# Kernel optimization log

Hardware: AMD Instinct MI355X
Metric: run time of the kernel (lower is better)

The kernel has to match this reference:

```python
import jax, jax.numpy as jnp
import numpy as np

N_PIX = 4_194_304      # native emulator wavelength grid length
N_BINS = 350_000       # number of data wavelength bins (searchsorted labels)
MEDIAN_WL = 10500.0    # Angstroms, np.median(wl_bin_edges)
C_KMS = 299792.458     # speed of light, km/s
PI_SRC = 3.1415926654  # the (slightly off) pi literal used in the source
KERNEL_TAPS = 901      # torch.arange(-4.5, 4.51, 0.01)


def _conv_same(flux, kernel):
    """conv1d with padding='same'; kernels are symmetric so corr == conv."""
    half = kernel.shape[0] // 2
    out = jax.lax.conv_general_dilated(
        flux[None, None, :], kernel[None, None, :],
        window_strides=(1,), padding=[(half, half)])
    return out[0, 0]


def setup_inputs() -> dict:
    key = jax.random.key(0)
    k1, k2 = jax.random.split(key)
    return {
        "high_res_model": jax.random.uniform(k1, (N_PIX,), dtype=jnp.float32),
        "ln_sigma_angs": jnp.asarray(-2.3, dtype=jnp.float32),
        "ln_vsini": jnp.asarray(2.89, dtype=jnp.float32),
        "segment_ids": jnp.sort(jax.random.randint(k2, (N_PIX,), 0, N_BINS)),
    }


def reference(high_res_model, ln_sigma_angs, ln_vsini, segment_ids):
    dt = high_res_model.dtype
    grid = jnp.linspace(-4.5, 4.5, KERNEL_TAPS).astype(dt)
    sigma_angs = 0.01 + jnp.exp(ln_sigma_angs)
    vsini = 0.9 + jnp.exp(ln_vsini)

    # --- rotational broadening kernel ---
    x = (C_KMS * grid / MEDIAN_WL) / vsini
    x2 = jnp.minimum(x * x, 1.0)                     # torch.clamp(x2, max=1)
    inside = x2 < 0.99999999
    safe_x2 = jnp.where(inside, x2, 0.0)             # avoid sqrt(neg)/nan-grad
    rot_kernel = jnp.where(inside, 2.0 * jnp.sqrt(1.0 - safe_x2), 0.0)
    rot_kernel = rot_kernel / jnp.sum(rot_kernel)
    rot = _conv_same(high_res_model, rot_kernel)

    # --- instrumental (Gaussian) broadening kernel ---
    gauss = (1.0 / (sigma_angs * jnp.sqrt(jnp.asarray(2.0 * PI_SRC, dt)))
             * jnp.exp(-0.5 * grid * grid / (sigma_angs * sigma_angs)) * 0.01)
    conv = _conv_same(rot, gauss)

    # --- resample to data: fused segment mean (replaces split+per-bin mean) ---
    sums = jax.ops.segment_sum(conv, segment_ids, num_segments=N_BINS)
    counts = jax.ops.segment_sum(jnp.ones_like(conv), segment_ids,
                                 num_segments=N_BINS)
    means = sums / jnp.maximum(counts, 1.0)
    return jnp.clip(means, 0.0, 1.0)[1:-1]
```

## Files before the change

### kernel.cpp

```cpp
#include <hip/hip_runtime.h>
#include <hip/hip_bf16.h>

#define TAPS 901
#define CB 256
#define R 15
#define NGRP 16
#define NK (R * NGRP)
#define OPB (CB * R)
#define TILE 4112

__device__ __forceinline__ float4 ld4(const float* p) {
  return *reinterpret_cast<const float4*>(p);
}

__global__ __launch_bounds__(1024) void prep(
    const float* __restrict__ lns, const float* __restrict__ lnv,
    const float* __restrict__ flux, const int* __restrict__ ids,
    float* __restrict__ comb_w, int* __restrict__ bounds,
    float* __restrict__ sums, int n) {
  __shared__ float rk[1024], gk[1024], red[1024];
  __shared__ float ck[2048];
  __shared__ int sb[8];
  const int t = threadIdx.x;
  if (t < 8) sb[t] = (t & 1) ? -1 : 4096;
  __syncthreads();

  const float sigma = 0.01f + expf(lns[0]);
  const float vsini = 0.9f + expf(lnv[0]);

  float rv = 0.f, gv = 0.f;
  if (t < TAPS) {
    float g = -4.5f + 0.01f * (float)t;
    float x = (299792.458f * g / 10500.0f) / vsini;
    float x2 = fminf(x * x, 1.0f);
    if (x2 < 1.0f) rv = 2.0f * sqrtf(1.0f - x2);
    gv = (1.0f / (sigma * sqrtf(2.0f * 3.1415926654f))) *
         expf(-0.5f * g * g / (sigma * sigma)) * 0.01f;
  }
  red[t] = rv;
  __syncthreads();
  for (int s = 512; s > 0; s >>= 1) {
    if (t < s) red[t] += red[t + s];
    __syncthreads();
  }
  const float rsum = red[0];

  const float rw = (t < TAPS) ? rv / rsum : 0.f;
  rk[t] = rw;
  gk[t] = gv;
  if (t < TAPS) {
    if (rw != 0.f)          { atomicMin(&sb[0], t); atomicMax(&sb[1], t); }
    if (fabsf(gv) > 1e-10f) { atomicMin(&sb[2], t); atomicMax(&sb[3], t); }
  }
  __syncthreads();
  const int rlo = sb[0], rhi = sb[1], glo = sb[2], ghi = sb[3];
  int flo = 450 - glo; if (flo < 0) flo = 0;
  int fhi = ghi - 450; if (fhi < 0) fhi = 0;

  if (blockIdx.x == 0) {
    for (int t2 = t; t2 < 2048; t2 += 1024) {
      float c = 0.f;
      if (t2 <= 1800) {
        int jmin = rlo > t2 - ghi ? rlo : t2 - ghi;
        int jmax = rhi < t2 - glo ? rhi : t2 - glo;
        for (int j = jmin; j <= jmax; ++j) c += rk[j] * gk[t2 - j];
      }
      ck[t2] = c;
      comb_w[t2] = c;
      if (t2 <= 1800 && fabsf(c) > 1e-12f) { atomicMin(&sb[4], t2); atomicMax(&sb[5], t2); }
    }
    __syncthreads();
    if (t == 0) {
      int clo = sb[4], chi = sb[5];
      if (chi < clo) { clo = 900; chi = 900; }
      while (chi - (clo & ~3) + 1 > NK) {
        if (fabsf(ck[clo]) <= fabsf(ck[chi])) ++clo; else --chi;
      }
      bounds[0] = clo & ~3; bounds[1] = flo; bounds[2] = fhi;
    }
  } else if (blockIdx.x == 1) {
    const int m = flo + fhi;
    float* rbuf = ck;
    for (int j = t; j < m; j += 1024) {
      float s = 0.f;
      int j0 = 450 - j > rlo ? 450 - j : rlo;
      for (int j2 = j0; j2 <= rhi; ++j2) s += rk[j2] * flux[j + j2 - 450];
      rbuf[j] = s;
    }
    __syncthreads();
    for (int i = t; i < flo; i += 1024) {
      float c = 0.f;
      int k0 = 450 - i > glo ? 450 - i : glo;
      for (int k = k0; k <= ghi; ++k) c += gk[k] * rbuf[i + k - 450];
      atomicAdd(&sums[ids[i]], c);
    }
  } else {
    const int m = flo + fhi;
    float* rbuf = ck;
    const int jbase = n - m;
    for (int jj = t; jj < m; jj += 1024) {
      int j = jbase + jj;
      float s = 0.f;
      int j2hi = n - 1 + 450 - j < rhi ? n - 1 + 450 - j : rhi;
      for (int j2 = rlo; j2 <= j2hi; ++j2) s += rk[j2] * flux[j + j2 - 450];
      rbuf[jj] = s;
    }
    __syncthreads();
    for (int ii = t; ii < fhi; ii += 1024) {
      int i = n - fhi + ii;
      float c = 0.f;
      int khi = n - 1 + 450 - i < ghi ? n - 1 + 450 - i : ghi;
      for (int k = glo; k <= khi; ++k) c += gk[k] * rbuf[i + k - 450 - jbase];
      atomicAdd(&sums[ids[i]], c);
    }
  }
}

__global__ __launch_bounds__(CB) void conv_scatter(
    const float* __restrict__ flux, const float* __restrict__ comb_w,
    const int* __restrict__ bounds, const int* __restrict__ ids,
    float* __restrict__ sums, int* __restrict__ bstart, int n, int nbins) {
  __shared__ __align__(16) float lds[TILE];
  __shared__ __align__(16) float wl[NGRP * 16];
  const int tid = threadIdx.x;
  const int clo4 = __builtin_amdgcn_readfirstlane(bounds[0]);
  const int flo  = __builtin_amdgcn_readfirstlane(bounds[1]);
  const int fhi  = __builtin_amdgcn_readfirstlane(bounds[2]);
  const int blockBase = blockIdx.x * OPB;
  const int start = blockBase - 900 + clo4;

  for (int j = tid * 4; j < OPB + NK; j += CB * 4) {
    int g = start + j;
    float4 v;
    if (g >= 0 && g + 3 < n) {
      v = ld4(flux + g);
    } else {
      v.x = (unsigned)g       < (unsigned)n ? flux[g]     : 0.f;
      v.y = (unsigned)(g + 1) < (unsigned)n ? flux[g + 1] : 0.f;
      v.z = (unsigned)(g + 2) < (unsigned)n ? flux[g + 2] : 0.f;
      v.w = (unsigned)(g + 3) < (unsigned)n ? flux[g + 3] : 0.f;
    }
    *reinterpret_cast<float4*>(&lds[j]) = v;
  }
  {
    const int g = tid >> 4, u = tid & 15;
    wl[tid] = (u < 15) ? comb_w[clo4 + g * 15 + u] : 0.f;
  }
  __syncthreads();

  const int idx0 = tid * R;
  float win[R];
#pragma unroll
  for (int r = 0; r < R; ++r) win[r] = lds[idx0 + r];
  float acc[R];
#pragma unroll
  for (int r = 0; r < R; ++r) acc[r] = 0.f;

  const float4* wl4 = reinterpret_cast<const float4*>(wl);
#define TAP(u, wv)                                                     \
  {                                                                    \
    _Pragma("unroll") for (int r = 0; r < R; ++r)                      \
        acc[r] = fmaf(wv, win[((u) + r) % R], acc[r]);                 \
    win[u] = lds[idx0 + kk + (u) + R];                                 \
  }
#pragma unroll 2
  for (int g = 0; g < NGRP; ++g) {
    const int kk = g * R;
    const float4 q0 = wl4[g * 4 + 0];
    const float4 q1 = wl4[g * 4 + 1];
    const float4 q2 = wl4[g * 4 + 2];
    const float4 q3 = wl4[g * 4 + 3];
    TAP(0, q0.x)  TAP(1, q0.y)  TAP(2, q0.z)  TAP(3, q0.w)
    TAP(4, q1.x)  TAP(5, q1.y)  TAP(6, q1.z)  TAP(7, q1.w)
    TAP(8, q2.x)  TAP(9, q2.y)  TAP(10, q2.z) TAP(11, q2.w)
    TAP(12, q3.x) TAP(13, q3.y) TAP(14, q3.z)
  }
#undef TAP

  const int base = blockBase + idx0;
  const int loskip = flo - base;
  const int hicap = (n - fhi) - base;
  int prev = (base > 0) ? ((base < n) ? ids[base - 1] : 0) : -1;
  int cur = -1; float run = 0.f;
#pragma unroll
  for (int r = 0; r < R; ++r) {
    const int p = base + r;
    if (p < n) {
      const int id = ids[p];
      if (id != prev) {
        for (int b = prev + 1; b <= id; ++b) bstart[b] = p;
        prev = id;
      }
      if (r >= loskip && r < hicap) {
        if (id == cur) {
          run += acc[r];
        } else {
          if (cur >= 0) atomicAdd(&sums[cur], run);
          cur = id; run = acc[r];
        }
      }
    }
  }
  if (cur >= 0) atomicAdd(&sums[cur], run);
  if (base < n && base + R > n - 1) {
    for (int b = prev + 1; b < nbins; ++b) bstart[b] = n;
  }
}

__global__ __launch_bounds__(256) void seg_mean(
    const float* __restrict__ sums, const int* __restrict__ bstart,
    float* __restrict__ out, int out_n) {
  const int gid = blockIdx.x * blockDim.x + threadIdx.x;
  if (gid >= out_n) return;
  const int b = gid + 1;
  const int c = bstart[b + 1] - bstart[b];
  const float mean = sums[b] / (float)(c > 1 ? c : 1);
  out[gid] = fminf(fmaxf(mean, 0.f), 1.f);
}

extern "C" void kernel_launch(void* const* d_in, const int* in_sizes, int n_in,
                              void* d_out, int out_size, void* d_ws,
                              size_t ws_size, hipStream_t stream) {
  const float* flux = (const float*)d_in[0];
  const float* lns  = (const float*)d_in[1];
  const float* lnv  = (const float*)d_in[2];
  const int*   ids  = (const int*)d_in[3];
  float* out = (float*)d_out;
  const int n = in_sizes[0];
  const int nbins = out_size + 2;

  float* ws      = (float*)d_ws;
  float* comb_w  = ws;
  int*   bounds  = (int*)(ws + 2048);
  float* sums    = ws + 2112;
  int*   bstart  = (int*)(sums + nbins);

  hipMemsetAsync(sums, 0, (size_t)nbins * sizeof(float), stream);
  prep<<<3, 1024, 0, stream>>>(lns, lnv, flux, ids, comb_w, bounds, sums, n);
  const int nblk = (n + OPB - 1) / OPB;
  conv_scatter<<<nblk, CB, 0, stream>>>(flux, comb_w, bounds, ids, sums,
                                        bstart, n, nbins);
  seg_mean<<<(out_size + 255) / 256, 256, 0, stream>>>(sums, bstart, out,
                                                       out_size);
}
```

Before: 141.2 us.

## Replace per-pixel convolution with prefix-sum bin dot products per segment

Rather than convolving every pixel and scatter-adding into bins, each block builds a prefix sum of its flux window in shared memory. Each bin's sum of convolved values is then computed directly as a weighted dot product of prefix differences with the combined kernel. This removes the global atomics and the separate mean kernel. Edge corrections are precomputed into a per-bin buffer and bin starts come from a separate kernel. The changes add more kernel launches and a serial chunked scan, and float prefix sums over thousands of elements can lose precision. The cost now scales with bins per block times taps instead of pixels times taps.

```diff
diff --git a/kernel.cpp b/kernel.cpp
--- a/kernel.cpp
+++ b/kernel.cpp
@@ -4,20 +4,14 @@
 #define TAPS 901
 #define CB 256
 #define R 15
-#define NGRP 16
-#define NK (R * NGRP)
+#define NK 240
 #define OPB (CB * R)
-#define TILE 4112
-
-__device__ __forceinline__ float4 ld4(const float* p) {
-  return *reinterpret_cast<const float4*>(p);
-}
-
-__global__ __launch_bounds__(1024) void prep(
+#define WL 4864
+#define CHUNK 19
+
+__global__ __launch_bounds__(1024) void prep0(
     const float* __restrict__ lns, const float* __restrict__ lnv,
-    const float* __restrict__ flux, const int* __restrict__ ids,
-    float* __restrict__ comb_w, int* __restrict__ bounds,
-    float* __restrict__ sums, int n) {
+    float* __restrict__ comb_w, int* __restrict__ bounds) {
   __shared__ float rk[1024], gk[1024], red[1024];
   __shared__ float ck[2048];
   __shared__ int sb[8];
@@ -54,33 +48,74 @@
   }
   __syncthreads();
   const int rlo = sb[0], rhi = sb[1], glo = sb[2], ghi = sb[3];
+
+  for (int t2 = t; t2 < 2048; t2 += 1024) {
+    float c = 0.f;
+    if (t2 <= 1800) {
+      int jmin = rlo > t2 - ghi ? rlo : t2 - ghi;
+      int jmax = rhi < t2 - glo ? rhi : t2 - glo;
+      for (int j = jmin; j <= jmax; ++j) c += rk[j] * gk[t2 - j];
+    }
+    ck[t2] = c;
+    comb_w[t2] = c;
+    if (t2 <= 1800 && fabsf(c) > 1e-12f) { atomicMin(&sb[4], t2); atomicMax(&sb[5], t2); }
+  }
+  __syncthreads();
+  if (t == 0) {
+    int clo = sb[4], chi = sb[5];
+    if (chi < clo) { clo = 900; chi = 900; }
+    while (chi - (clo & ~3) + 1 > NK) {
+      if (fabsf(ck[clo]) <= fabsf(ck[chi])) ++clo; else --chi;
+    }
+    int flo = 450 - glo; if (flo < 0) flo = 0;
+    int fhi = ghi - 450; if (fhi < 0) fhi = 0;
+    bounds[0] = clo & ~3; bounds[1] = flo; bounds[2] = fhi;
+  }
+}
+
+__global__ __launch_bounds__(1024) void prep1(
+    const float* __restrict__ lns, const float* __restrict__ lnv,
+    const float* __restrict__ flux, const int* __restrict__ ids,
+    const float* __restrict__ comb_w, const int* __restrict__ bounds,
+    float* __restrict__ edgeCorr, int n) {
+  __shared__ float rk[1024], gk[1024], red[1024], rbuf[928];
+  __shared__ int sb[4];
+  const int t = threadIdx.x;
+  if (t < 4) sb[t] = (t & 1) ? -1 : 4096;
+  __syncthreads();
+
+  const float sigma = 0.01f + expf(lns[0]);
+  const float vsini = 0.9f + expf(lnv[0]);
+  float rv = 0.f, gv = 0.f;
+  if (t < TAPS) {
+    float g = -4.5f + 0.01f * (float)t;
+    float x = (299792.458f * g / 10500.0f) / vsini;
+    float x2 = fminf(x * x, 1.0f);
+    if (x2 < 1.0f) rv = 2.0f * sqrtf(1.0f - x2);
+    gv = (1.0f / (sigma * sqrtf(2.0f * 3.1415926654f))) *
+         expf(-0.5f * g * g / (sigma * sigma)) * 0.01f;
+  }
+  red[t] = rv;
+  __syncthreads();
+  for (int s = 512; s > 0; s >>= 1) {
+    if (t < s) red[t] += red[t + s];
+    __syncthreads();
+  }
+  const float rsum = red[0];
+  rk[t] = (t < TAPS) ? rv / rsum : 0.f;
+  gk[t] = gv;
+  if (t < TAPS) {
+    if (rk[t] != 0.f)       { atomicMin(&sb[0], t); atomicMax(&sb[1], t); }
+    if (fabsf(gv) > 1e-10f) { atomicMin(&sb[2], t); atomicMax(&sb[3], t); }
+  }
+  __syncthreads();
+  const int rlo = sb[0], rhi = sb[1], glo = sb[2], ghi = sb[3];
   int flo = 450 - glo; if (flo < 0) flo = 0;
   int fhi = ghi - 450; if (fhi < 0) fhi = 0;
+  const int m = flo + fhi;
+  const int clo4 = bounds[0];
 
   if (blockIdx.x == 0) {
-    for (int t2 = t; t2 < 2048; t2 += 1024) {
-      float c = 0.f;
-      if (t2 <= 1800) {
-        int jmin = rlo > t2 - ghi ? rlo : t2 - ghi;
-        int jmax = rhi < t2 - glo ? rhi : t2 - glo;
-        for (int j = jmin; j <= jmax; ++j) c += rk[j] * gk[t2 - j];
-      }
-      ck[t2] = c;
-      comb_w[t2] = c;
-      if (t2 <= 1800 && fabsf(c) > 1e-12f) { atomicMin(&sb[4], t2); atomicMax(&sb[5], t2); }
-    }
-    __syncthreads();
-    if (t == 0) {
-      int clo = sb[4], chi = sb[5];
-      if (chi < clo) { clo = 900; chi = 900; }
-      while (chi - (clo & ~3) + 1 > NK) {
-        if (fabsf(ck[clo]) <= fabsf(ck[chi])) ++clo; else --chi;
-      }
-      bounds[0] = clo & ~3; bounds[1] = flo; bounds[2] = fhi;
-    }
-  } else if (blockIdx.x == 1) {
-    const int m = flo + fhi;
-    float* rbuf = ck;
     for (int j = t; j < m; j += 1024) {
       float s = 0.f;
       int j0 = 450 - j > rlo ? 450 - j : rlo;
@@ -89,14 +124,17 @@
     }
     __syncthreads();
     for (int i = t; i < flo; i += 1024) {
-      float c = 0.f;
+      float ex = 0.f;
       int k0 = 450 - i > glo ? 450 - i : glo;
-      for (int k = k0; k <= ghi; ++k) c += gk[k] * rbuf[i + k - 450];
-      atomicAdd(&sums[ids[i]], c);
+      for (int k = k0; k <= ghi; ++k) ex += gk[k] * rbuf[i + k - 450];
+      float cb = 0.f;
+      for (int t2 = 0; t2 < NK; ++t2) {
+        int q = i + clo4 + t2 - 900;
+        if (q >= 0 && q < n) cb = fmaf(comb_w[clo4 + t2], flux[q], cb);
+      }
+      atomicAdd(&edgeCorr[ids[i]], ex - cb);
     }
   } else {
-    const int m = flo + fhi;
-    float* rbuf = ck;
     const int jbase = n - m;
     for (int jj = t; jj < m; jj += 1024) {
       int j = jbase + jj;
@@ -108,114 +146,113 @@
     __syncthreads();
     for (int ii = t; ii < fhi; ii += 1024) {
       int i = n - fhi + ii;
-      float c = 0.f;
+      float ex = 0.f;
       int khi = n - 1 + 450 - i < ghi ? n - 1 + 450 - i : ghi;
-      for (int k = glo; k <= khi; ++k) c += gk[k] * rbuf[i + k - 450 - jbase];
-      atomicAdd(&sums[ids[i]], c);
-    }
-  }
-}
-
-__global__ __launch_bounds__(CB) void conv_scatter(
+      for (int k = glo; k <= khi; ++k) ex += gk[k] * rbuf[i + k - 450 - jbase];
+      float cb = 0.f;
+      for (int t2 = 0; t2 < NK; ++t2) {
+        int q = i + clo4 + t2 - 900;
+        if (q >= 0 && q < n) cb = fmaf(comb_w[clo4 + t2], flux[q], cb);
+      }
+      atomicAdd(&edgeCorr[ids[i]], ex - cb);
+    }
+  }
+}
+
+__global__ __launch_bounds__(256) void build_bstart(
+    const int* __restrict__ ids, int* __restrict__ bstart, int n, int nbins) {
+  const int gid = blockIdx.x * 256 + threadIdx.x;
+  const int p0 = gid * 8;
+  if (p0 >= n) return;
+  int prev = (p0 == 0) ? -1 : ids[p0 - 1];
+  const int4 a = *reinterpret_cast<const int4*>(ids + p0);
+  const int4 b4 = *reinterpret_cast<const int4*>(ids + p0 + 4);
+  const int v[8] = {a.x, a.y, a.z, a.w, b4.x, b4.y, b4.z, b4.w};
+#pragma unroll
+  for (int r = 0; r < 8; ++r) {
+    const int id = v[r];
+    if (id != prev) {
+      for (int b = prev + 1; b <= id; ++b) bstart[b] = p0 + r;
+      prev = id;
+    }
+  }
+  if (p0 + 8 >= n) {
+    for (int b = prev + 1; b <= nbins; ++b) bstart[b] = n;
+  }
+}
+
+__global__ __launch_bounds__(CB) void bin_dot(
     const float* __restrict__ flux, const float* __restrict__ comb_w,
     const int* __restrict__ bounds, const int* __restrict__ ids,
-    float* __restrict__ sums, int* __restrict__ bstart, int n, int nbins) {
-  __shared__ __align__(16) float lds[TILE];
-  __shared__ __align__(16) float wl[NGRP * 16];
+    const int* __restrict__ bstart, const float* __restrict__ edgeCorr,
+    float* __restrict__ out, int n, int nbins) {
+  __shared__ float W[WL];
+  __shared__ float wl[NK];
+  __shared__ float caux[CB];
   const int tid = threadIdx.x;
   const int clo4 = __builtin_amdgcn_readfirstlane(bounds[0]);
-  const int flo  = __builtin_amdgcn_readfirstlane(bounds[1]);
-  const int fhi  = __builtin_amdgcn_readfirstlane(bounds[2]);
   const int blockBase = blockIdx.x * OPB;
-  const int start = blockBase - 900 + clo4;
-
-  for (int j = tid * 4; j < OPB + NK; j += CB * 4) {
-    int g = start + j;
-    float4 v;
-    if (g >= 0 && g + 3 < n) {
-      v = ld4(flux + g);
+  const int wstart = blockBase - 900 + clo4;
+
+  if (tid == 0) W[0] = 0.f;
+  for (int j = tid; j < WL - 1; j += CB) {
+    const int g = wstart + j;
+    W[1 + j] = ((unsigned)g < (unsigned)n) ? flux[g] : 0.f;
+  }
+  if (tid < NK) wl[tid] = comb_w[clo4 + tid];
+  __syncthreads();
+
+  {
+    const int base = 1 + tid * CHUNK;
+    const int lim = min(base + CHUNK, WL);
+    float s = 0.f;
+    for (int j = base; j < lim; ++j) { s += W[j]; W[j] = s; }
+    caux[tid] = s;
+    __syncthreads();
+    for (int off = 1; off < CB; off <<= 1) {
+      const float v = (tid >= off) ? caux[tid - off] : 0.f;
+      __syncthreads();
+      caux[tid] += v;
+      __syncthreads();
+    }
+    const float offv = (tid == 0) ? 0.f : caux[tid - 1];
+    for (int j = base; j < lim; ++j) W[j] += offv;
+  }
+  __syncthreads();
+
+  const int blo = (blockBase == 0) ? 0 : ids[blockBase - 1] + 1;
+  const int lastpix = min(blockBase + OPB, n) - 1;
+  int bhi = ids[lastpix];
+  if (blockBase + OPB >= n) bhi = nbins - 1;
+  const int oe_last = bstart[bhi + 1] - blockBase;
+  const bool fallback = (oe_last + NK > WL);
+
+  for (int b = blo + tid; b <= bhi; b += CB) {
+    const int s = bstart[b], e = bstart[b + 1];
+    float a0 = 0.f, a1 = 0.f, a2 = 0.f, a3 = 0.f;
+    if (!fallback) {
+      const int os = s - blockBase, oe = e - blockBase;
+#pragma unroll 4
+      for (int t2 = 0; t2 < NK; t2 += 4) {
+        a0 = fmaf(wl[t2 + 0], W[oe + t2 + 0] - W[os + t2 + 0], a0);
+        a1 = fmaf(wl[t2 + 1], W[oe + t2 + 1] - W[os + t2 + 1], a1);
+        a2 = fmaf(wl[t2 + 2], W[oe + t2 + 2] - W[os + t2 + 2], a2);
+        a3 = fmaf(wl[t2 + 3], W[oe + t2 + 3] - W[os + t2 + 3], a3);
+      }
     } else {
-      v.x = (unsigned)g       < (unsigned)n ? flux[g]     : 0.f;
-      v.y = (unsigned)(g + 1) < (unsigned)n ? flux[g + 1] : 0.f;
-      v.z = (unsigned)(g + 2) < (unsigned)n ? flux[g + 2] : 0.f;
-      v.w = (unsigned)(g + 3) < (unsigned)n ? flux[g + 3] : 0.f;
-    }
-    *reinterpret_cast<float4*>(&lds[j]) = v;
-  }
-  {
-    const int g = tid >> 4, u = tid & 15;
-    wl[tid] = (u < 15) ? comb_w[clo4 + g * 15 + u] : 0.f;
-  }
-  __syncthreads();
-
-  const int idx0 = tid * R;
-  float win[R];
-#pragma unroll
-  for (int r = 0; r < R; ++r) win[r] = lds[idx0 + r];
-  float acc[R];
-#pragma unroll
-  for (int r = 0; r < R; ++r) acc[r] = 0.f;
-
-  const float4* wl4 = reinterpret_cast<const float4*>(wl);
-#define TAP(u, wv)                                                     \
-  {                                                                    \
-    _Pragma("unroll") for (int r = 0; r < R; ++r)                      \
-        acc[r] = fmaf(wv, win[((u) + r) % R], acc[r]);                 \
-    win[u] = lds[idx0 + kk + (u) + R];                                 \
-  }
-#pragma unroll 2
-  for (int g = 0; g < NGRP; ++g) {
-    const int kk = g * R;
-    const float4 q0 = wl4[g * 4 + 0];
-    const float4 q1 = wl4[g * 4 + 1];
-    const float4 q2 = wl4[g * 4 + 2];
-    const float4 q3 = wl4[g * 4 + 3];
-    TAP(0, q0.x)  TAP(1, q0.y)  TAP(2, q0.z)  TAP(3, q0.w)
-    TAP(4, q1.x)  TAP(5, q1.y)  TAP(6, q1.z)  TAP(7, q1.w)
-    TAP(8, q2.x)  TAP(9, q2.y)  TAP(10, q2.z) TAP(11, q2.w)
-    TAP(12, q3.x) TAP(13, q3.y) TAP(14, q3.z)
-  }
-#undef TAP
-
-  const int base = blockBase + idx0;
-  const int loskip = flo - base;
-  const int hicap = (n - fhi) - base;
-  int prev = (base > 0) ? ((base < n) ? ids[base - 1] : 0) : -1;
-  int cur = -1; float run = 0.f;
-#pragma unroll
-  for (int r = 0; r < R; ++r) {
-    const int p = base + r;
-    if (p < n) {
-      const int id = ids[p];
-      if (id != prev) {
-        for (int b = prev + 1; b <= id; ++b) bstart[b] = p;
-        prev = id;
-      }
-      if (r >= loskip && r < hicap) {
-        if (id == cur) {
-          run += acc[r];
-        } else {
-          if (cur >= 0) atomicAdd(&sums[cur], run);
-          cur = id; run = acc[r];
+      for (int i = s; i < e; ++i)
+        for (int t2 = 0; t2 < NK; ++t2) {
+          const int q = i + clo4 + t2 - 900;
+          if ((unsigned)q < (unsigned)n) a0 = fmaf(wl[t2], flux[q], a0);
         }
-      }
-    }
-  }
-  if (cur >= 0) atomicAdd(&sums[cur], run);
-  if (base < n && base + R > n - 1) {
-    for (int b = prev + 1; b < nbins; ++b) bstart[b] = n;
-  }
-}
-
-__global__ __launch_bounds__(256) void seg_mean(
-    const float* __restrict__ sums, const int* __restrict__ bstart,
-    float* __restrict__ out, int out_n) {
-  const int gid = blockIdx.x * blockDim.x + threadIdx.x;
-  if (gid >= out_n) return;
-  const int b = gid + 1;
-  const int c = bstart[b + 1] - bstart[b];
-  const float mean = sums[b] / (float)(c > 1 ? c : 1);
-  out[gid] = fminf(fmaxf(mean, 0.f), 1.f);
+    }
+    const float sum = ((a0 + a1) + (a2 + a3)) + edgeCorr[b];
+    if (b >= 1 && b <= nbins - 2) {
+      const int c = e - s;
+      const float mean = sum / (float)(c > 1 ? c : 1);
+      out[b - 1] = fminf(fmaxf(mean, 0.f), 1.f);
+    }
+  }
 }
 
 extern "C" void kernel_launch(void* const* d_in, const int* in_sizes, int n_in,
@@ -229,17 +266,18 @@
   const int n = in_sizes[0];
   const int nbins = out_size + 2;
 
-  float* ws      = (float*)d_ws;
-  float* comb_w  = ws;
-  int*   bounds  = (int*)(ws + 2048);
-  float* sums    = ws + 2112;
-  int*   bstart  = (int*)(sums + nbins);
-
-  hipMemsetAsync(sums, 0, (size_t)nbins * sizeof(float), stream);
-  prep<<<3, 1024, 0, stream>>>(lns, lnv, flux, ids, comb_w, bounds, sums, n);
+  float* ws       = (float*)d_ws;
+  float* comb_w   = ws;
+  int*   bounds   = (int*)(ws + 2048);
+  float* edgeCorr = ws + 2112;
+  int*   bstart   = (int*)(edgeCorr + nbins);
+
+  hipMemsetAsync(edgeCorr, 0, (size_t)nbins * sizeof(float), stream);
+  prep0<<<1, 1024, 0, stream>>>(lns, lnv, comb_w, bounds);
+  prep1<<<2, 1024, 0, stream>>>(lns, lnv, flux, ids, comb_w, bounds,
+                                edgeCorr, n);
+  build_bstart<<<(n / 8 + 255) / 256, 256, 0, stream>>>(ids, bstart, n, nbins);
   const int nblk = (n + OPB - 1) / OPB;
-  conv_scatter<<<nblk, CB, 0, stream>>>(flux, comb_w, bounds, ids, sums,
-                                        bstart, n, nbins);
-  seg_mean<<<(out_size + 255) / 256, 256, 0, stream>>>(sums, bstart, out,
-                                                       out_size);
-}
+  bin_dot<<<nblk, CB, 0, stream>>>(flux, comb_w, bounds, ids, bstart,
+                                   edgeCorr, out, n, nbins);
+}
```

New measurement: 201.0 us. 42.4% more time.
